# Optimization experiments

Hardware: AMD Instinct MI355X
Metric: run time of the kernel (lower is better)

Reference implementation:

```python
import jax, jax.numpy as jnp
import numpy as np

ALPHA = 0.95       # synaptic decay for layers l>0
BETA = 0.9         # membrane decay
THRESHOLD = 1.0
RESET = 0.0        # reset_potential
SIM_T = 100        # simulation_time
SG_SCALE = 100.0   # SuperSpike surrogate-gradient scale (SurrGradSpike)

@jax.custom_vjp
def spike(x):
    # forward: Heaviside step on (mem - threshold)
    return (x > 0).astype(x.dtype)

def _spike_fwd(x):
    return spike(x), x

def _spike_bwd(x, g):
    # SuperSpike surrogate: grad / (scale*|x| + 1)^2
    return (g / (SG_SCALE * jnp.abs(x) + 1.0) ** 2,)

spike.defvjp(_spike_fwd, _spike_bwd)


def setup_inputs() -> dict:
    key = jax.random.key(0)
    k1, k2, k3 = jax.random.split(key, 3)
    B, D, H = 256, 1024, 2048
    inputs = jax.random.normal(k1, (B, D), dtype=jnp.float32)
    w0 = jax.random.normal(k2, (D, H), dtype=jnp.float32) / np.sqrt(D).astype(np.float32)
    w1 = jax.random.normal(k3, (H, H), dtype=jnp.float32) / np.sqrt(H).astype(np.float32)
    return {"inputs": inputs, "w0": w0, "w1": w1}


def _simulate(inputs, w0, w1):
    B = inputs.shape[0]
    H0, H1 = w0.shape[1], w1.shape[1]
    # torch code does inputs.detach().clone() each step -> no grad to inputs
    x = jax.lax.stop_gradient(inputs)

    def step(carry, _):
        s0, m0, s1, m1 = carry
        # layer 0: new_syn = 0*syn + input @ W0
        ns0 = x @ w0
        nm0 = BETA * m0 + ns0
        mthr = nm0 - THRESHOLD          # hidden (non-final) layer spikes
        z = spike(mthr)
        nm0 = jnp.where(mthr > 0, RESET, nm0)   # masked reset after spike
        # layer 1 (final, non-spiking readout): new_syn = alpha*syn + z @ W1
        ns1 = ALPHA * s1 + z @ w1
        nm1 = BETA * m1 + ns1
        return (ns0, nm0, ns1, nm1), (nm0, nm1, z)

    init = (jnp.zeros((B, H0), jnp.float32), jnp.zeros((B, H0), jnp.float32),
            jnp.zeros((B, H1), jnp.float32), jnp.zeros((B, H1), jnp.float32))
    # torch loop records zeros at t==0 and updates for t=1..T-1
    _, (mem0_rec, mem1_rec, spk_rec) = jax.lax.scan(step, init, None, length=SIM_T - 1)
    z0 = jnp.zeros((1, B, H0), jnp.float32)
    z1 = jnp.zeros((1, B, H1), jnp.float32)
    mem0_rec = jnp.concatenate([z0, mem0_rec], axis=0)   # [T, B, H0]
    mem1_rec = jnp.concatenate([z1, mem1_rec], axis=0)   # [T, B, H1]
    spk_rec = jnp.concatenate([z0, spk_rec], axis=0)     # [T, B, H0]
    mem_rec = jnp.stack([mem0_rec, mem1_rec], axis=1)    # [T, L=2, B, H]
    return mem1_rec[-1], mem_rec, spk_rec


def reference(inputs, w0, w1):
    # returns (mem_rec[-1][-1], mem_rec, spk_rec) like the torch module
    return _simulate(inputs, w0, w1)
```

## Files before the change

### kernel.cpp

```cpp
#include <hip/hip_runtime.h>
#include <hip/hip_bf16.h>

#define Bdim 256
#define Ddim 1024
#define Hdim 2048
#define Tdim 100
#define BH (Bdim*Hdim)
#define M3 ((Tdim-1)*Bdim)
#define ZB8 ((size_t)M3*Hdim)

#define OUT_MEM ((size_t)BH)
#define OUT_SPK ((size_t)BH + (size_t)Tdim*2*BH)

typedef __attribute__((ext_vector_type(8))) short short8;
typedef __attribute__((ext_vector_type(4))) float f32x4;
typedef __attribute__((ext_vector_type(4))) int   i32x4;

#define GLD16(g, l) __builtin_amdgcn_global_load_lds( \
    (__attribute__((address_space(1))) void*)(g), \
    (__attribute__((address_space(3))) void*)(l), 16, 0, 0)

static __device__ __forceinline__ unsigned short bf16bits(float f) {
  __hip_bfloat16 h = __float2bfloat16(f);
  return *reinterpret_cast<unsigned short*>(&h);
}

__global__ __launch_bounds__(256) void kcvt_split(const float* __restrict__ X,
                                                  unsigned short* __restrict__ Xhi,
                                                  unsigned short* __restrict__ Xlo) {
  int i = (blockIdx.x*256 + threadIdx.x)*4;
  float4 v = *reinterpret_cast<const float4*>(&X[i]);
  ushort4 ph, pl;
  float f, fh;
  f = v.x; { __hip_bfloat16 h = __float2bfloat16(f); fh = __bfloat162float(h); ph.x = *reinterpret_cast<unsigned short*>(&h); } pl.x = bf16bits(f - fh);
  f = v.y; { __hip_bfloat16 h = __float2bfloat16(f); fh = __bfloat162float(h); ph.y = *reinterpret_cast<unsigned short*>(&h); } pl.y = bf16bits(f - fh);
  f = v.z; { __hip_bfloat16 h = __float2bfloat16(f); fh = __bfloat162float(h); ph.z = *reinterpret_cast<unsigned short*>(&h); } pl.z = bf16bits(f - fh);
  f = v.w; { __hip_bfloat16 h = __float2bfloat16(f); fh = __bfloat162float(h); ph.w = *reinterpret_cast<unsigned short*>(&h); } pl.w = bf16bits(f - fh);
  *reinterpret_cast<ushort4*>(&Xhi[i]) = ph;
  *reinterpret_cast<ushort4*>(&Xlo[i]) = pl;
}

__global__ __launch_bounds__(256) void ktr_split(const float* __restrict__ In,
                                                 unsigned short* __restrict__ OutHi,
                                                 unsigned short* __restrict__ OutLo,
                                                 int R, int C) {
  __shared__ unsigned short thi[32][33];
  __shared__ unsigned short tlo[32][33];
  int bk = blockIdx.x*32, bn = blockIdx.y*32;
  int tx = threadIdx.x & 31, ty = threadIdx.x >> 5;
  for (int r = ty; r < 32; r += 8) {
    float f = In[(size_t)(bk + r)*C + bn + tx];
    __hip_bfloat16 h = __float2bfloat16(f);
    float fh = __bfloat162float(h);
    thi[r][tx] = *reinterpret_cast<unsigned short*>(&h);
    tlo[r][tx] = bf16bits(f - fh);
  }
  __syncthreads();
  for (int r = ty; r < 32; r += 8) {
    OutHi[(size_t)(bn + r)*R + bk + tx] = thi[tx][r];
    OutLo[(size_t)(bn + r)*R + bk + tx] = tlo[tx][r];
  }
}

__global__ __launch_bounds__(256) void kcolmax_part(const float* __restrict__ W1,
                                                    float* __restrict__ pmax) {
  int n = blockIdx.x*256 + threadIdx.x;
  int kc = blockIdx.y;
  float m = 0.f;
  #pragma unroll 8
  for (int k = kc*64; k < kc*64 + 64; ++k)
    m = fmaxf(m, fabsf(W1[(size_t)k*Hdim + n]));
  pmax[(size_t)kc*Hdim + n] = m;
}

__global__ __launch_bounds__(256) void kcolmax_fin(const float* __restrict__ pmax,
                                                   float* __restrict__ scales) {
  int n = blockIdx.x*256 + threadIdx.x;
  float m = 0.f;
  #pragma unroll
  for (int i = 0; i < 32; ++i)
    m = fmaxf(m, pmax[(size_t)i*Hdim + n]);
  scales[n] = m * (1.0f/127.0f);
}

__global__ __launch_bounds__(256) void ktr_i8(const float* __restrict__ In,
                                              const float* __restrict__ scales,
                                              signed char* __restrict__ Out) {
  __shared__ signed char tile[32][33];
  int bk = blockIdx.x*32, bn = blockIdx.y*32;
  int tx = threadIdx.x & 31, ty = threadIdx.x >> 5;
  float rs = 1.0f / scales[bn + tx];
  for (int r = ty; r < 32; r += 8)
    tile[r][tx] = (signed char)(int)rintf(In[(size_t)(bk + r)*Hdim + bn + tx] * rs);
  __syncthreads();
  for (int r = ty; r < 32; r += 8)
    Out[(size_t)(bn + r)*Hdim + bk + tx] = tile[tx][r];
}

#define K1F_NK 32
__global__ __launch_bounds__(256) void k1_fused(const unsigned short* __restrict__ xhi,
                                                const unsigned short* __restrict__ xlo,
                                                const unsigned short* __restrict__ whiT,
                                                const unsigned short* __restrict__ wloT,
                                                float* __restrict__ NS0) {
  __shared__ short Ah[2][64*32], Al[2][64*32];
  __shared__ short Bh[2][64*32], Bl[2][64*32];
  int tid = threadIdx.x;
  int l = tid & 63, w = tid >> 6;
  int wm = w >> 1, wn = w & 1;
  int lr = l & 15, lg = l >> 4;
  size_t gm = (size_t)blockIdx.x * 64;
  size_t gn = (size_t)blockIdx.y * 64;
  int srow = l >> 2;
  int scol = ((l & 3)*8) ^ (((l >> 2) & 6) << 2);
  const unsigned short* gah = &xhi [(gm + w*16 + srow)*1024 + scol];
  const unsigned short* gal = &xlo [(gm + w*16 + srow)*1024 + scol];
  const unsigned short* gbh = &whiT[(gn + w*16 + srow)*1024 + scol];
  const unsigned short* gbl = &wloT[(gn + w*16 + srow)*1024 + scol];
  int rdswz = (lr & 6) << 2;
  f32x4 acc[2][2] = {};
  GLD16(gah, &Ah[0][w*512]); GLD16(gal, &Al[0][w*512]);
  GLD16(gbh, &Bh[0][w*512]); GLD16(gbl, &Bl[0][w*512]);
  __syncthreads();
  #pragma unroll 2
  for (int t = 0; t < K1F_NK; ++t) {
    int cur = t & 1;
    if (t + 1 < K1F_NK) {
      int nxt = cur ^ 1; size_t ko = (size_t)(t + 1)*32;
      GLD16(gah + ko, &Ah[nxt][w*512]); GLD16(gal + ko, &Al[nxt][w*512]);
      GLD16(gbh + ko, &Bh[nxt][w*512]); GLD16(gbl + ko, &Bl[nxt][w*512]);
    }
    short8 ah[2], al[2], bh[2], bl[2];
    #pragma unroll
    for (int mi = 0; mi < 2; ++mi) {
      int ro = (wm*32 + mi*16 + lr)*32 + (lg*8 ^ rdswz);
      ah[mi] = *reinterpret_cast<const short8*>(&Ah[cur][ro]);
      al[mi] = *reinterpret_cast<const short8*>(&Al[cur][ro]);
    }
    #pragma unroll
    for (int ni = 0; ni < 2; ++ni) {
      int ro = (wn*32 + ni*16 + lr)*32 + (lg*8 ^ rdswz);
      bh[ni] = *reinterpret_cast<const short8*>(&Bh[cur][ro]);
      bl[ni] = *reinterpret_cast<const short8*>(&Bl[cur][ro]);
    }
    #pragma unroll
    for (int mi = 0; mi < 2; ++mi)
      #pragma unroll
      for (int ni = 0; ni < 2; ++ni) {
        acc[mi][ni] = __builtin_amdgcn_mfma_f32_16x16x32_bf16(ah[mi], bh[ni], acc[mi][ni], 0, 0, 0);
        acc[mi][ni] = __builtin_amdgcn_mfma_f32_16x16x32_bf16(ah[mi], bl[ni], acc[mi][ni], 0, 0, 0);
        acc[mi][ni] = __builtin_amdgcn_mfma_f32_16x16x32_bf16(al[mi], bh[ni], acc[mi][ni], 0, 0, 0);
      }
    __syncthreads();
  }
  #pragma unroll
  for (int mi = 0; mi < 2; ++mi)
    #pragma unroll
    for (int ni = 0; ni < 2; ++ni)
      #pragma unroll
      for (int q = 0; q < 4; ++q)
        NS0[(gm + wm*32 + mi*16 + lg*4 + q)*Hdim + gn + wn*32 + ni*16 + lr] = acc[mi][ni][q];
}

__global__ __launch_bounds__(256) void k2_sim(const float* __restrict__ NS0,
                                              float* __restrict__ out,
                                              signed char* __restrict__ Zb) {
  size_t i4 = ((size_t)blockIdx.x*256 + threadIdx.x)*4;
  float4 nsv = *reinterpret_cast<const float4*>(&NS0[i4]);
  float ns[4] = {nsv.x, nsv.y, nsv.z, nsv.w};
  float* mem = out + OUT_MEM;
  float* spk = out + OUT_SPK;
  float4 z4 = {0.f, 0.f, 0.f, 0.f};
  *reinterpret_cast<float4*>(&mem[i4]) = z4;
  *reinterpret_cast<float4*>(&mem[BH + i4]) = z4;
  *reinterpret_cast<float4*>(&spk[i4]) = z4;
  float m[4] = {0.f, 0.f, 0.f, 0.f};
  for (int t = 1; t < Tdim; ++t) {
    float4 mo, zf; uchar4 z8;
    #pragma unroll
    for (int j = 0; j < 4; ++j) {
      m[j] = __fadd_rn(__fmul_rn(0.9f, m[j]), ns[j]);
      bool sp = m[j] > 1.0f;
      if (sp) m[j] = 0.f;
      ((float*)&mo)[j] = m[j];
      ((float*)&zf)[j] = sp ? 1.f : 0.f;
      ((unsigned char*)&z8)[j] = sp ? (unsigned char)1 : (unsigned char)0;
    }
    *reinterpret_cast<float4*>(&mem[(size_t)(2*t)*BH + i4]) = mo;
    *reinterpret_cast<float4*>(&spk[(size_t)t*BH + i4]) = zf;
    *reinterpret_cast<uchar4*>(&Zb[(size_t)(t-1)*BH + i4]) = z8;
  }
}

#define NKT3 32

#define K3_ST(g, ldsarr, half, kt) \
  GLD16((g) + (size_t)(kt)*64 + (size_t)(half)*128*2048, &ldsarr[(kt)&1][(half)*8192 + w*1024])

#define K3_LDA(h) do { \
  _Pragma("unroll") \
  for (int mi = 0; mi < 4; ++mi) \
    af[mi] = *reinterpret_cast<const i32x4*>( \
      &As[bb][((h)*128 + wm*64 + mi*16 + lr)*64 + ((lg ^ rxa)<<4)]); \
} while(0)

#define K3_LDB(v, bf) do { \
  _Pragma("unroll") \
  for (int ni = 0; ni < 2; ++ni) \
    bf[ni] = *reinterpret_cast<const i32x4*>( \
      &Bs[bb][((v)*128 + wn*32 + ni*16 + lr)*64 + ((lg ^ rxa)<<4)]); \
} while(0)

#define K3_MFMA(h, v, bf) do { \
  __builtin_amdgcn_s_setprio(1); \
  _Pragma("unroll") \
  for (int mi = 0; mi < 4; ++mi) \
    _Pragma("unroll") \
    for (int ni = 0; ni < 2; ++ni) \
      acc[(h)*4+mi][(v)*2+ni] = __builtin_amdgcn_mfma_i32_16x16x64_i8(af[mi], bf[ni], acc[(h)*4+mi][(v)*2+ni], 0, 0, 0); \
  __builtin_amdgcn_s_setprio(0); \
} while(0)

template<int CB>
__global__ __launch_bounds__(512, 2) void k3_gemm(const signed char* __restrict__ A,
                                                  const signed char* __restrict__ BT,
                                                  const float* __restrict__ scales,
                                                  float* __restrict__ mem1,
                                                  unsigned short* __restrict__ cbuf) {
  __shared__ signed char As[2][256*64];
  __shared__ signed char Bs[2][256*64];
  int tid = threadIdx.x;
  int l = tid & 63;
  int w = tid >> 6;
  int wm = w >> 2, wn = w & 3;
  int lr = l & 15, lg = l >> 4;
  int rxa = (lr >> 1) & 3;

  int lin = blockIdx.x;
  int wg = (lin & 7)*99 + (lin >> 3);
  int mtile = wg >> 3, ntile = wg & 7;
  size_t gm = (size_t)mtile * 256;
  size_t gn = (size_t)ntile * 256;

  int srow = l >> 2;
  int scol = ((l & 3) ^ ((l >> 3) & 3)) << 4;
  const signed char* gA = &A [(gm + w*16 + srow)*2048 + scol];
  const signed char* gB = &BT[(gn + w*16 + srow)*2048 + scol];

  i32x4 acc[8][4] = {};

  K3_ST(gA, As, 0, 0); K3_ST(gA, As, 1, 0);
  K3_ST(gB, Bs, 0, 0); K3_ST(gB, Bs, 1, 0);
  asm volatile("s_waitcnt vmcnt(0)" ::: "memory");
  __builtin_amdgcn_s_barrier();
  asm volatile("" ::: "memory");

  for (int kt = 0; kt < NKT3; ++kt) {
    int bb = kt & 1;
    if (kt + 1 < NKT3) {
      K3_ST(gA, As, 0, kt + 1); K3_ST(gA, As, 1, kt + 1);
      K3_ST(gB, Bs, 0, kt + 1); K3_ST(gB, Bs, 1, kt + 1);
    }
    i32x4 af[4], bfl[2], bfh[2];
    K3_LDA(0); K3_LDB(0, bfl); K3_LDB(1, bfh);
    K3_MFMA(0, 0, bfl);
    K3_MFMA(0, 1, bfh);
    K3_LDA(1);
    K3_MFMA(1, 0, bfl);
    K3_MFMA(1, 1, bfh);
    asm volatile("s_waitcnt vmcnt(0)" ::: "memory");
    __builtin_amdgcn_s_barrier();
    asm volatile("" ::: "memory");
  }

  float sc[2][2];
  #pragma unroll
  for (int vv = 0; vv < 2; ++vv)
    #pragma unroll
    for (int ni = 0; ni < 2; ++ni)
      sc[vv][ni] = scales[gn + vv*128 + wn*32 + ni*16 + lr];

  if (CB) {
    unsigned short* cp = cbuf + (size_t)mtile*BH + gn;
    #pragma unroll
    for (int hh = 0; hh < 2; ++hh)
      #pragma unroll
      for (int mi = 0; mi < 4; ++mi)
        #pragma unroll
        for (int vv = 0; vv < 2; ++vv)
          #pragma unroll
          for (int ni = 0; ni < 2; ++ni)
            #pragma unroll
            for (int q = 0; q < 4; ++q) {
              int b   = hh*128 + wm*64 + mi*16 + lg*4 + q;
              int col = vv*128 + wn*32 + ni*16 + lr;
              cp[(size_t)b*Hdim + col] =
                bf16bits((float)acc[hh*4+mi][vv*2+ni][q] * sc[vv][ni]);
            }
  } else {
    float* plane = mem1 + (size_t)(2*mtile + 3)*BH + gn;
    #pragma unroll
    for (int hh = 0; hh < 2; ++hh)
      #pragma unroll
      for (int mi = 0; mi < 4; ++mi)
        #pragma unroll
        for (int vv = 0; vv < 2; ++vv)
          #pragma unroll
          for (int ni = 0; ni < 2; ++ni)
            #pragma unroll
            for (int q = 0; q < 4; ++q) {
              int b   = hh*128 + wm*64 + mi*16 + lg*4 + q;
              int col = vv*128 + wn*32 + ni*16 + lr;
              plane[(size_t)b*Hdim + col] =
                (float)acc[hh*4+mi][vv*2+ni][q] * sc[vv][ni];
            }
  }
}

__global__ __launch_bounds__(256) void k4_rec(float* __restrict__ out) {
  size_t i4 = ((size_t)blockIdx.x*256 + threadIdx.x)*4;
  float* mem = out + OUT_MEM;
  float s[4] = {0.f,0.f,0.f,0.f}, m[4] = {0.f,0.f,0.f,0.f};
  for (int t = 1; t < Tdim; ++t) {
    float4* p = reinterpret_cast<float4*>(&mem[(size_t)(2*t + 1)*BH + i4]);
    float4 c = *p;
    float4 mo;
    #pragma unroll
    for (int j = 0; j < 4; ++j) {
      s[j] = __fadd_rn(__fmul_rn(0.95f, s[j]), ((float*)&c)[j]);
      m[j] = __fadd_rn(__fmul_rn(0.9f, m[j]), s[j]);
      ((float*)&mo)[j] = m[j];
    }
    *p = mo;
  }
  float4 o = {m[0], m[1], m[2], m[3]};
  *reinterpret_cast<float4*>(&out[i4]) = o;
}

__global__ __launch_bounds__(256) void k4_rec_cb(const unsigned short* __restrict__ C,
                                                 float* __restrict__ out) {
  size_t i4 = ((size_t)blockIdx.x*256 + threadIdx.x)*4;
  float* mem = out + OUT_MEM;
  float s[4] = {0.f,0.f,0.f,0.f}, m[4] = {0.f,0.f,0.f,0.f};
  for (int t = 1; t < Tdim; ++t) {
    ushort4 cv = *reinterpret_cast<const ushort4*>(&C[(size_t)(t-1)*BH + i4]);
    float4 mo;
    #pragma unroll
    for (int j = 0; j < 4; ++j) {
      unsigned int u = ((unsigned short*)&cv)[j];
      float c = __uint_as_float(u << 16);
      s[j] = __fadd_rn(__fmul_rn(0.95f, s[j]), c);
      m[j] = __fadd_rn(__fmul_rn(0.9f, m[j]), s[j]);
      ((float*)&mo)[j] = m[j];
    }
    *reinterpret_cast<float4*>(&mem[(size_t)(2*t + 1)*BH + i4]) = mo;
  }
  float4 o = {m[0], m[1], m[2], m[3]};
  *reinterpret_cast<float4*>(&out[i4]) = o;
}

extern "C" void kernel_launch(void* const* d_in, const int* in_sizes, int n_in,
                              void* d_out, int out_size, void* d_ws, size_t ws_size,
                              hipStream_t stream) {
  const float* X  = (const float*)d_in[0];
  const float* W0 = (const float*)d_in[1];
  const float* W1 = (const float*)d_in[2];
  float* out = (float*)d_out;
  char* ws = (char*)d_ws;

  float*          ns0    = (float*)ws;
  signed char*    w1t8   = (signed char*)(ws + (2ull << 20));
  float*          scales = (float*)(ws + (6ull << 20));
  float*          pmax   = (float*)(ws + (6ull << 20) + (64ull << 10));
  signed char*    zb     = (signed char*)(ws + (10ull << 20));
  unsigned short* cbuf   = (unsigned short*)(ws + (10ull << 20) + ZB8);
  size_t needCb = (10ull << 20) + ZB8 + (size_t)M3*Hdim*2;
  int useCb = (ws_size >= needCb) ? 1 : 0;
  unsigned short* xhi = (unsigned short*)(ws + (10ull << 20));
  unsigned short* xlo = (unsigned short*)(ws + (10ull << 20) + (512<<10));
  unsigned short* whi = (unsigned short*)(ws + (11ull << 20));
  unsigned short* wlo = (unsigned short*)(ws + (15ull << 20));

  kcvt_split  <<<dim3(256),     256, 0, stream>>>(X, xhi, xlo);
  ktr_split   <<<dim3(32, 64),  256, 0, stream>>>(W0, whi, wlo, 1024, 2048);
  kcolmax_part<<<dim3(8, 32),   256, 0, stream>>>(W1, pmax);
  kcolmax_fin <<<dim3(8),       256, 0, stream>>>(pmax, scales);
  ktr_i8      <<<dim3(64, 64),  256, 0, stream>>>(W1, scales, w1t8);
  k1_fused    <<<dim3(4, 32),   256, 0, stream>>>(xhi, xlo, whi, wlo, ns0);
  k2_sim      <<<dim3(BH/1024), 256, 0, stream>>>(ns0, out, zb);
  if (useCb) {
    k3_gemm<1><<<dim3((M3/256)*(Hdim/256)), 512, 0, stream>>>(zb, w1t8, scales, out + OUT_MEM, cbuf);
    k4_rec_cb<<<dim3(BH/1024), 256, 0, stream>>>(cbuf, out);
  } else {
    k3_gemm<0><<<dim3((M3/256)*(Hdim/256)), 512, 0, stream>>>(zb, w1t8, scales, out + OUT_MEM, cbuf);
    k4_rec  <<<dim3(BH/1024), 256, 0, stream>>>(out);
  }
}
```

Measured before the change: 403.2 us.

## Shrink int8 GEMM tile to 256x128 with triple-buffered LDS pipeline

The int8 spike×W1 GEMM tile shrinks from 256x256 to 256x128, which doubles the block count, halves the accumulators per thread and raises the occupancy target to 4 blocks per CU. The LDS ring grows to three buffers, so loads run two K-steps ahead with a partial vmcnt wait instead of a full drain every iteration. The intent is better latency hiding and more resident waves. The cost is more redundant reads of A and lower arithmetic intensity per tile.

After: 361.4 us (median of 2 runs). 10.4% less time.

```diff
diff --git a/kernel.cpp b/kernel.cpp
--- a/kernel.cpp
+++ b/kernel.cpp
@@ -194,126 +194,103 @@
 
 #define NKT3 32
 
-#define K3_ST(g, ldsarr, half, kt) \
-  GLD16((g) + (size_t)(kt)*64 + (size_t)(half)*128*2048, &ldsarr[(kt)&1][(half)*8192 + w*1024])
-
-#define K3_LDA(h) do { \
-  _Pragma("unroll") \
-  for (int mi = 0; mi < 4; ++mi) \
-    af[mi] = *reinterpret_cast<const i32x4*>( \
-      &As[bb][((h)*128 + wm*64 + mi*16 + lr)*64 + ((lg ^ rxa)<<4)]); \
-} while(0)
-
-#define K3_LDB(v, bf) do { \
-  _Pragma("unroll") \
-  for (int ni = 0; ni < 2; ++ni) \
-    bf[ni] = *reinterpret_cast<const i32x4*>( \
-      &Bs[bb][((v)*128 + wn*32 + ni*16 + lr)*64 + ((lg ^ rxa)<<4)]); \
-} while(0)
-
-#define K3_MFMA(h, v, bf) do { \
-  __builtin_amdgcn_s_setprio(1); \
-  _Pragma("unroll") \
-  for (int mi = 0; mi < 4; ++mi) \
-    _Pragma("unroll") \
-    for (int ni = 0; ni < 2; ++ni) \
-      acc[(h)*4+mi][(v)*2+ni] = __builtin_amdgcn_mfma_i32_16x16x64_i8(af[mi], bf[ni], acc[(h)*4+mi][(v)*2+ni], 0, 0, 0); \
-  __builtin_amdgcn_s_setprio(0); \
-} while(0)
-
 template<int CB>
-__global__ __launch_bounds__(512, 2) void k3_gemm(const signed char* __restrict__ A,
+__global__ __launch_bounds__(512, 4) void k3_gemm(const signed char* __restrict__ A,
                                                   const signed char* __restrict__ BT,
                                                   const float* __restrict__ scales,
                                                   float* __restrict__ mem1,
                                                   unsigned short* __restrict__ cbuf) {
-  __shared__ signed char As[2][256*64];
-  __shared__ signed char Bs[2][256*64];
+  __shared__ signed char As[3][256*64];
+  __shared__ signed char Bs[3][128*64];
   int tid = threadIdx.x;
   int l = tid & 63;
   int w = tid >> 6;
-  int wm = w >> 2, wn = w & 3;
+  int wm = w >> 1, wn = w & 1;
   int lr = l & 15, lg = l >> 4;
   int rxa = (lr >> 1) & 3;
 
   int lin = blockIdx.x;
-  int wg = (lin & 7)*99 + (lin >> 3);
-  int mtile = wg >> 3, ntile = wg & 7;
+  int wg = (lin & 7)*198 + (lin >> 3);
+  int mtile = wg >> 4, ntile = wg & 15;
   size_t gm = (size_t)mtile * 256;
-  size_t gn = (size_t)ntile * 256;
+  size_t gn = (size_t)ntile * 128;
 
   int srow = l >> 2;
   int scol = ((l & 3) ^ ((l >> 3) & 3)) << 4;
-  const signed char* gA = &A [(gm + w*16 + srow)*2048 + scol];
-  const signed char* gB = &BT[(gn + w*16 + srow)*2048 + scol];
-
-  i32x4 acc[8][4] = {};
-
-  K3_ST(gA, As, 0, 0); K3_ST(gA, As, 1, 0);
-  K3_ST(gB, Bs, 0, 0); K3_ST(gB, Bs, 1, 0);
-  asm volatile("s_waitcnt vmcnt(0)" ::: "memory");
-  __builtin_amdgcn_s_barrier();
-  asm volatile("" ::: "memory");
-
+  const signed char* gA0 = &A [(gm +       w*16 + srow)*2048 + scol];
+  const signed char* gA1 = &A [(gm + 128 + w*16 + srow)*2048 + scol];
+  const signed char* gB  = &BT[(gn +       w*16 + srow)*2048 + scol];
+
+  #define K3_ST(kt, buf) do { size_t _ko = (size_t)(kt)*64;  \
+      GLD16(gA0 + _ko, &As[buf][w*1024]);                     \
+      GLD16(gA1 + _ko, &As[buf][8192 + w*1024]);              \
+      GLD16(gB  + _ko, &Bs[buf][w*1024]); } while (0)
+
+  i32x4 acc[4][4] = {};
+
+  K3_ST(0, 0);
+  K3_ST(1, 1);
+
+  int bb = 0;
   for (int kt = 0; kt < NKT3; ++kt) {
-    int bb = kt & 1;
-    if (kt + 1 < NKT3) {
-      K3_ST(gA, As, 0, kt + 1); K3_ST(gA, As, 1, kt + 1);
-      K3_ST(gB, Bs, 0, kt + 1); K3_ST(gB, Bs, 1, kt + 1);
-    }
-    i32x4 af[4], bfl[2], bfh[2];
-    K3_LDA(0); K3_LDB(0, bfl); K3_LDB(1, bfh);
-    K3_MFMA(0, 0, bfl);
-    K3_MFMA(0, 1, bfh);
-    K3_LDA(1);
-    K3_MFMA(1, 0, bfl);
-    K3_MFMA(1, 1, bfh);
-    asm volatile("s_waitcnt vmcnt(0)" ::: "memory");
+    if (kt == NKT3 - 1) asm volatile("s_waitcnt vmcnt(0)" ::: "memory");
+    else                asm volatile("s_waitcnt vmcnt(3)" ::: "memory");
     __builtin_amdgcn_s_barrier();
     asm volatile("" ::: "memory");
-  }
-
-  float sc[2][2];
+
+    int b2 = bb + 2; if (b2 >= 3) b2 -= 3;
+    if (kt + 2 < NKT3) K3_ST(kt + 2, b2);
+
+    i32x4 af[4], bf[4];
+    #pragma unroll
+    for (int mi = 0; mi < 4; ++mi)
+      af[mi] = *reinterpret_cast<const i32x4*>(
+        &As[bb][(wm*64 + mi*16 + lr)*64 + ((lg ^ rxa)<<4)]);
+    #pragma unroll
+    for (int ni = 0; ni < 4; ++ni)
+      bf[ni] = *reinterpret_cast<const i32x4*>(
+        &Bs[bb][(wn*64 + ni*16 + lr)*64 + ((lg ^ rxa)<<4)]);
+    __builtin_amdgcn_s_setprio(1);
+    #pragma unroll
+    for (int mi = 0; mi < 4; ++mi)
+      #pragma unroll
+      for (int ni = 0; ni < 4; ++ni)
+        acc[mi][ni] = __builtin_amdgcn_mfma_i32_16x16x64_i8(af[mi], bf[ni], acc[mi][ni], 0, 0, 0);
+    __builtin_amdgcn_s_setprio(0);
+
+    ++bb; if (bb >= 3) bb -= 3;
+  }
+  #undef K3_ST
+
+  float sc[4];
   #pragma unroll
-  for (int vv = 0; vv < 2; ++vv)
-    #pragma unroll
-    for (int ni = 0; ni < 2; ++ni)
-      sc[vv][ni] = scales[gn + vv*128 + wn*32 + ni*16 + lr];
+  for (int ni = 0; ni < 4; ++ni)
+    sc[ni] = scales[gn + wn*64 + ni*16 + lr];
 
   if (CB) {
     unsigned short* cp = cbuf + (size_t)mtile*BH + gn;
     #pragma unroll
-    for (int hh = 0; hh < 2; ++hh)
-      #pragma unroll
-      for (int mi = 0; mi < 4; ++mi)
+    for (int mi = 0; mi < 4; ++mi)
+      #pragma unroll
+      for (int ni = 0; ni < 4; ++ni)
         #pragma unroll
-        for (int vv = 0; vv < 2; ++vv)
-          #pragma unroll
-          for (int ni = 0; ni < 2; ++ni)
-            #pragma unroll
-            for (int q = 0; q < 4; ++q) {
-              int b   = hh*128 + wm*64 + mi*16 + lg*4 + q;
-              int col = vv*128 + wn*32 + ni*16 + lr;
-              cp[(size_t)b*Hdim + col] =
-                bf16bits((float)acc[hh*4+mi][vv*2+ni][q] * sc[vv][ni]);
-            }
+        for (int q = 0; q < 4; ++q) {
+          int b   = wm*64 + mi*16 + lg*4 + q;
+          int col = wn*64 + ni*16 + lr;
+          cp[(size_t)b*Hdim + col] = bf16bits((float)acc[mi][ni][q] * sc[ni]);
+        }
   } else {
     float* plane = mem1 + (size_t)(2*mtile + 3)*BH + gn;
     #pragma unroll
-    for (int hh = 0; hh < 2; ++hh)
-      #pragma unroll
-      for (int mi = 0; mi < 4; ++mi)
+    for (int mi = 0; mi < 4; ++mi)
+      #pragma unroll
+      for (int ni = 0; ni < 4; ++ni)
         #pragma unroll
-        for (int vv = 0; vv < 2; ++vv)
-          #pragma unroll
-          for (int ni = 0; ni < 2; ++ni)
-            #pragma unroll
-            for (int q = 0; q < 4; ++q) {
-              int b   = hh*128 + wm*64 + mi*16 + lg*4 + q;
-              int col = vv*128 + wn*32 + ni*16 + lr;
-              plane[(size_t)b*Hdim + col] =
-                (float)acc[hh*4+mi][vv*2+ni][q] * sc[vv][ni];
-            }
+        for (int q = 0; q < 4; ++q) {
+          int b   = wm*64 + mi*16 + lg*4 + q;
+          int col = wn*64 + ni*16 + lr;
+          plane[(size_t)b*Hdim + col] = (float)acc[mi][ni][q] * sc[ni];
+        }
   }
 }
 
@@ -389,10 +366,10 @@
   k1_fused    <<<dim3(4, 32),   256, 0, stream>>>(xhi, xlo, whi, wlo, ns0);
   k2_sim      <<<dim3(BH/1024), 256, 0, stream>>>(ns0, out, zb);
   if (useCb) {
-    k3_gemm<1><<<dim3((M3/256)*(Hdim/256)), 512, 0, stream>>>(zb, w1t8, scales, out + OUT_MEM, cbuf);
+    k3_gemm<1><<<dim3((M3/256)*(Hdim/128)), 512, 0, stream>>>(zb, w1t8, scales, out + OUT_MEM, cbuf);
     k4_rec_cb<<<dim3(BH/1024), 256, 0, stream>>>(cbuf, out);
   } else {
-    k3_gemm<0><<<dim3((M3/256)*(Hdim/256)), 512, 0, stream>>>(zb, w1t8, scales, out + OUT_MEM, cbuf);
+    k3_gemm<0><<<dim3((M3/256)*(Hdim/128)), 512, 0, stream>>>(zb, w1t8, scales, out + OUT_MEM, cbuf);
     k4_rec  <<<dim3(BH/1024), 256, 0, stream>>>(out);
   }
 }
```
